# Performance work log

Hardware: AMD Instinct MI355X
Metric: run time of the kernel (lower is better)

The kernel has to match this reference:

```python
import jax, jax.numpy as jnp
import numpy as np

N_NODES = 20000
N_EDGES = 320000
IN_DIM = 256
HIDDEN = 256
OUT_DIM = 128
N_LAYERS = 3
N_GROUPS = 4
EXP_PER_GROUP = 2
N_EXPERTS = N_GROUPS * EXP_PER_GROUP
TOP_K = 2


def setup_inputs() -> dict:
    key = jax.random.key(0)
    ks = jax.random.split(key, 12)
    d = HIDDEN
    r = 2 * d  # router/expert input dim: concat(node, neighbor-mean)
    x = jax.random.normal(ks[0], (N_NODES, IN_DIM), dtype=jnp.float32)
    edge_index = jax.random.randint(ks[1], (2, N_EDGES), 0, N_NODES, dtype=jnp.int32)
    s = 0.05
    Wg = jax.random.normal(ks[2], (N_LAYERS, r, N_GROUPS), dtype=jnp.float32) * s
    We = jax.random.normal(ks[3], (N_LAYERS, r, N_EXPERTS), dtype=jnp.float32) * s
    Ww = jax.random.normal(ks[4], (N_LAYERS, r, d), dtype=jnp.float32) * s
    W1 = jax.random.normal(ks[5], (N_LAYERS, N_EXPERTS, r, d), dtype=jnp.float32) * s
    b1 = jnp.zeros((N_LAYERS, N_EXPERTS, d), dtype=jnp.float32)
    W2 = jax.random.normal(ks[6], (N_LAYERS, N_EXPERTS, d, d), dtype=jnp.float32) * s
    b2 = jnp.zeros((N_LAYERS, N_EXPERTS, d), dtype=jnp.float32)
    wc = jax.random.normal(ks[7], (N_LAYERS, r, 1), dtype=jnp.float32) * s
    Wout = jax.random.normal(ks[8], (d, OUT_DIM), dtype=jnp.float32) * s
    return {"x": x, "edge_index": edge_index, "Wg": Wg, "We": We, "Ww": Ww,
            "W1": W1, "b1": b1, "W2": W2, "b2": b2, "wc": wc, "Wout": Wout}


def _moe_layer(h, src, dst, deg, Wg, We, Ww, W1, b1, W2, b2, wc):
    N = h.shape[0]
    # graph message passing: mean aggregation over incoming edges
    agg = jax.ops.segment_sum(h[src], dst, num_segments=N) / deg  # [N, d]
    r = jnp.concatenate([h, agg], axis=-1)  # [N, 2d] combined router input
    # hierarchical routing: group softmax x within-group expert softmax
    gp = jax.nn.softmax(r @ Wg, axis=-1)                                # [N, G]
    ep = jax.nn.softmax((r @ We).reshape(N, N_GROUPS, EXP_PER_GROUP), axis=-1)
    probs = (gp[..., None] * ep).reshape(N, N_EXPERTS)                  # [N, E]
    # top-k gating, renormalized
    topv, topi = jax.lax.top_k(probs, TOP_K)
    gates = jnp.zeros_like(probs).at[jnp.arange(N)[:, None], topi].set(topv)
    gates = gates / (gates.sum(-1, keepdims=True) + 1e-9)              # [N, E]
    # strong experts: per-expert 2-layer MLP, combined by gates
    hid = jax.nn.relu(jnp.einsum('nf,efd->ned', r, W1) + b1[None])      # [N, E, d]
    exp_out = jnp.einsum('ned,edo->neo', hid, W2) + b2[None]            # [N, E, d]
    strong = jnp.einsum('ne,neo->no', gates, exp_out)                   # [N, d]
    # weak shared expert + confidence gate blend
    weak = r @ Ww                                                       # [N, d]
    conf = jax.nn.sigmoid(r @ wc)                                       # [N, 1]
    return jax.nn.relu(conf * strong + (1.0 - conf) * weak)


def reference(x, edge_index, Wg, We, Ww, W1, b1, W2, b2, wc, Wout):
    src, dst = edge_index[0], edge_index[1]
    N = x.shape[0]
    deg = jax.ops.segment_sum(jnp.ones((edge_index.shape[1],), jnp.float32), dst,
                              num_segments=N)
    deg = jnp.maximum(deg, 1.0)[:, None]
    h = x
    for l in range(Wg.shape[0]):  # small fixed layer loop
        h = _moe_layer(h, src, dst, deg, Wg[l], We[l], Ww[l],
                       W1[l], b1[l], W2[l], b2[l], wc[l])
    return h @ Wout
```

## Files before the change

kernel.cpp:

```cpp
#include <hip/hip_runtime.h>

#define NN 20000
#define NEDGE 320000
#define D 256
#define RD 512
#define OD 128
#define NEXP 8
#define NSLOT (2*NN)
#define NODE_BLOCKS 79
#define ASSIGN_BLOCKS 157

typedef unsigned short u16;
typedef __attribute__((ext_vector_type(4))) short short4v;
typedef __attribute__((ext_vector_type(8))) short short8v;
typedef __attribute__((ext_vector_type(16))) float f32x16;

__device__ __forceinline__ void split1(float v, u16& h, u16& m, u16& l) {
    unsigned b = __float_as_uint(v);
    h = (u16)(b >> 16);
    float fh = __uint_as_float(b & 0xffff0000u);
    float r1 = v - fh;
    unsigned b1 = __float_as_uint(r1);
    m = (u16)(b1 >> 16);
    float fm = __uint_as_float(b1 & 0xffff0000u);
    float r2 = r1 - fm;
    l = (u16)(__float_as_uint(r2) >> 16);
}


__global__ void copy_x_zero_cnt_k(const float* __restrict__ x, float* __restrict__ r,
                                  int* __restrict__ cnt) {
    int gid = blockIdx.x * 256 + threadIdx.x;
    int n = gid >> 6;
    int c4 = gid & 63;
    if (gid < NN * (D / 4)) {
        float4 v = reinterpret_cast<const float4*>(x)[gid];
        reinterpret_cast<float4*>(r + (size_t)n * RD)[c4] = v;
    }
    if (gid < NN) cnt[gid] = 0;
}

__global__ void count_edges_k(const int* __restrict__ dst, int* __restrict__ cnt) {
    int e = blockIdx.x * 256 + threadIdx.x;
    if (e < NEDGE) atomicAdd(&cnt[dst[e]], 1);
}

__global__ void block_sums_k(const int* __restrict__ cnt, int* __restrict__ bsum) {
    __shared__ int s[256];
    int i = blockIdx.x * 256 + threadIdx.x;
    s[threadIdx.x] = (i < NN) ? cnt[i] : 0;
    __syncthreads();
    for (int off = 128; off > 0; off >>= 1) {
        if (threadIdx.x < off) s[threadIdx.x] += s[threadIdx.x + off];
        __syncthreads();
    }
    if (threadIdx.x == 0) bsum[blockIdx.x] = s[0];
}

__global__ void scan_bsums_k(int* __restrict__ bsum, int* __restrict__ row_start) {
    if (blockIdx.x == 0 && threadIdx.x == 0) {
        int acc = 0;
        for (int i = 0; i < NODE_BLOCKS; i++) { int t = bsum[i]; bsum[i] = acc; acc += t; }
        row_start[NN] = acc;
    }
}

__global__ void block_scan_k(const int* __restrict__ cnt, const int* __restrict__ bsum,
                             int* __restrict__ row_start, int* __restrict__ cur) {
    __shared__ int s[256];
    int i = blockIdx.x * 256 + threadIdx.x;
    int v = (i < NN) ? cnt[i] : 0;
    s[threadIdx.x] = v;
    __syncthreads();
    for (int off = 1; off < 256; off <<= 1) {
        int t = (threadIdx.x >= off) ? s[threadIdx.x - off] : 0;
        __syncthreads();
        s[threadIdx.x] += t;
        __syncthreads();
    }
    int excl = s[threadIdx.x] - v + bsum[blockIdx.x];
    if (i < NN) { row_start[i] = excl; cur[i] = excl; }
}

__global__ void fill_csr_k(const int* __restrict__ src, const int* __restrict__ dst,
                           int* __restrict__ cur, int* __restrict__ csr_src) {
    int e = blockIdx.x * 256 + threadIdx.x;
    if (e < NEDGE) {
        int pos = atomicAdd(&cur[dst[e]], 1);
        csr_src[pos] = src[e];
    }
}

__global__ void aggregate_k(float* __restrict__ r, const int* __restrict__ row_start,
                            const int* __restrict__ csr_src, int* __restrict__ ec) {
    if (blockIdx.x == 0 && threadIdx.x < 16) ec[threadIdx.x] = 0;
    int wid = blockIdx.x * 4 + (threadIdx.x >> 6);
    int lane = threadIdx.x & 63;
    if (wid >= NN) return;
    int beg = row_start[wid], end = row_start[wid + 1];
    float ax = 0.f, ay = 0.f, az = 0.f, aw = 0.f;
    for (int j = beg; j < end; j++) {
        int s = csr_src[j];
        float4 v = reinterpret_cast<const float4*>(r + (size_t)s * RD)[lane];
        ax += v.x; ay += v.y; az += v.z; aw += v.w;
    }
    float deg = (float)((end - beg) > 1 ? (end - beg) : 1);
    float4 o = make_float4(ax / deg, ay / deg, az / deg, aw / deg);
    reinterpret_cast<float4*>(r + (size_t)wid * RD + D)[lane] = o;
}

__global__ void router_k(const float* __restrict__ r, const float* __restrict__ Wg,
                         const float* __restrict__ We, const float* __restrict__ wc,
                         int* __restrict__ node_top, float* __restrict__ node_gate,
                         float* __restrict__ conf) {
    int wid = blockIdx.x * 4 + (threadIdx.x >> 6);
    int lane = threadIdx.x & 63;
    if (wid >= NN) return;

    const float* rrow = r + (size_t)wid * RD;
    float pg[4] = {0, 0, 0, 0};
    float pe[8] = {0, 0, 0, 0, 0, 0, 0, 0};
    float pc = 0.f;
#pragma unroll
    for (int i = 0; i < 8; i++) {
        int k = lane + i * 64;
        float rv = rrow[k];
        float4 wg = *reinterpret_cast<const float4*>(Wg + (size_t)k * 4);
        pg[0] = fmaf(rv, wg.x, pg[0]); pg[1] = fmaf(rv, wg.y, pg[1]);
        pg[2] = fmaf(rv, wg.z, pg[2]); pg[3] = fmaf(rv, wg.w, pg[3]);
        float4 w0 = *reinterpret_cast<const float4*>(We + (size_t)k * 8);
        float4 w1 = *reinterpret_cast<const float4*>(We + (size_t)k * 8 + 4);
        pe[0] = fmaf(rv, w0.x, pe[0]); pe[1] = fmaf(rv, w0.y, pe[1]);
        pe[2] = fmaf(rv, w0.z, pe[2]); pe[3] = fmaf(rv, w0.w, pe[3]);
        pe[4] = fmaf(rv, w1.x, pe[4]); pe[5] = fmaf(rv, w1.y, pe[5]);
        pe[6] = fmaf(rv, w1.z, pe[6]); pe[7] = fmaf(rv, w1.w, pe[7]);
        pc = fmaf(rv, wc[k], pc);
    }
#pragma unroll
    for (int off = 32; off > 0; off >>= 1) {
#pragma unroll
        for (int g = 0; g < 4; g++) pg[g] += __shfl_xor(pg[g], off);
#pragma unroll
        for (int g = 0; g < 8; g++) pe[g] += __shfl_xor(pe[g], off);
        pc += __shfl_xor(pc, off);
    }

    if (lane == 0) {
        float m = fmaxf(fmaxf(pg[0], pg[1]), fmaxf(pg[2], pg[3]));
        float eg[4]; float sg = 0.f;
#pragma unroll
        for (int g = 0; g < 4; g++) { eg[g] = expf(pg[g] - m); sg += eg[g]; }
        float probs[8];
#pragma unroll
        for (int g = 0; g < 4; g++) {
            float a = pe[2 * g], b = pe[2 * g + 1];
            float mm = fmaxf(a, b);
            float ea = expf(a - mm), eb = expf(b - mm);
            float inv = 1.f / (ea + eb);
            float gp = eg[g] / sg;
            probs[2 * g]     = gp * ea * inv;
            probs[2 * g + 1] = gp * eb * inv;
        }
        int i0 = 0; float v0 = probs[0];
#pragma unroll
        for (int j = 1; j < 8; j++) if (probs[j] > v0) { v0 = probs[j]; i0 = j; }
        int i1 = -1; float v1 = -1e30f;
#pragma unroll
        for (int j = 0; j < 8; j++) if (j != i0 && probs[j] > v1) { v1 = probs[j]; i1 = j; }
        float s = v0 + v1 + 1e-9f;
        node_top[2 * wid] = i0;  node_top[2 * wid + 1] = i1;
        node_gate[2 * wid] = v0 / s;  node_gate[2 * wid + 1] = v1 / s;
        conf[wid] = 1.f / (1.f + expf(-pc));
    }
}

__global__ void expert_hist_k(const int* __restrict__ node_top, int* __restrict__ ec) {
    __shared__ int h[NEXP];
    if (threadIdx.x < NEXP) h[threadIdx.x] = 0;
    __syncthreads();
    int i = blockIdx.x * 256 + threadIdx.x;
    if (i < NSLOT) atomicAdd(&h[node_top[i]], 1);
    __syncthreads();
    if (threadIdx.x < NEXP && h[threadIdx.x] > 0) atomicAdd(&ec[threadIdx.x], h[threadIdx.x]);
}

__global__ void expert_scan_k(const int* __restrict__ ec, int* __restrict__ es,
                              int* __restrict__ ecur) {
    if (blockIdx.x == 0 && threadIdx.x == 0) {
        int acc = 0;
        for (int e = 0; e < NEXP; e++) { es[e] = acc; acc += ec[e]; ecur[e] = 0; }
        es[NEXP] = acc;
    }
}

__global__ void fill_experts_k(const int* __restrict__ node_top, const float* __restrict__ node_gate,
                               const int* __restrict__ es, int* __restrict__ ecur,
                               int* __restrict__ slot_node, float* __restrict__ slot_gate,
                               int* __restrict__ node_slot) {
    __shared__ int hcnt[NEXP], hbase[NEXP];
    int tid = threadIdx.x;
    if (tid < NEXP) hcnt[tid] = 0;
    __syncthreads();
    int i = blockIdx.x * 256 + tid;
    int e = 0, local = 0;
    bool act = (i < NSLOT);
    if (act) {
        e = node_top[i];
        local = atomicAdd(&hcnt[e], 1);
    }
    __syncthreads();
    if (tid < NEXP) hbase[tid] = (hcnt[tid] > 0) ? atomicAdd(&ecur[tid], hcnt[tid]) : 0;
    __syncthreads();
    if (act) {
        int slot = es[e] + hbase[e] + local;
        slot_node[slot] = i >> 1;
        slot_gate[slot] = node_gate[i];
        node_slot[i] = slot;
    }
}

__global__ void combine_k(const float* __restrict__ expout, const float* __restrict__ weak,
                          const float* __restrict__ conf, const int* __restrict__ node_slot,
                          float* __restrict__ r) {
    int gid = blockIdx.x * 256 + threadIdx.x;
    if (gid >= NN * (D / 4)) return;
    int n = gid >> 6, c4 = gid & 63;
    int s0 = node_slot[2 * n], s1 = node_slot[2 * n + 1];
    float4 e0 = reinterpret_cast<const float4*>(expout + (size_t)s0 * D)[c4];
    float4 e1 = reinterpret_cast<const float4*>(expout + (size_t)s1 * D)[c4];
    float4 w  = reinterpret_cast<const float4*>(weak + (size_t)n * D)[c4];
    float cf = conf[n], cg = 1.f - cf;
    float4 o;
    o.x = fmaxf(cf * (e0.x + e1.x) + cg * w.x, 0.f);
    o.y = fmaxf(cf * (e0.y + e1.y) + cg * w.y, 0.f);
    o.z = fmaxf(cf * (e0.z + e1.z) + cg * w.z, 0.f);
    o.w = fmaxf(cf * (e0.w + e1.w) + cg * w.w, 0.f);
    reinterpret_cast<float4*>(r + (size_t)n * RD)[c4] = o;
}

__global__ void btile_k(const float* __restrict__ src, u16* __restrict__ dH,
                        u16* __restrict__ dM, u16* __restrict__ dL,
                        int K, int N, int total) {
    int gid = blockIdx.x * 256 + threadIdx.x;
    if (gid >= total) return;
    int l = gid & 63;
    int tile = gid >> 6;
    int K16 = K >> 4;
    int kb = tile % K16;
    int t2 = tile / K16;
    int N32 = N >> 5;
    int nb = t2 % N32;
    int mat = t2 / N32;
    int kbase = (kb << 4) + ((l >> 5) << 3);
    int n = (nb << 5) + (l & 31);
    const float* s = src + ((size_t)mat * K + kbase) * N + n;
    short8v vh, vm, vl;
#pragma unroll
    for (int j = 0; j < 8; j++) {
        u16 hh, mm, ll;
        split1(s[(size_t)j * N], hh, mm, ll);
        vh[j] = (short)hh; vm[j] = (short)mm; vl[j] = (short)ll;
    }
    size_t o = (size_t)gid * 8;
    *reinterpret_cast<short8v*>(dH + o) = vh;
    *reinterpret_cast<short8v*>(dM + o) = vm;
    *reinterpret_cast<short8v*>(dL + o) = vl;
}

template <int MODE>
__global__ __launch_bounds__(256, 5) void gemm_mfma(
    const float* __restrict__ A, int lda,
    const u16* __restrict__ BH, const u16* __restrict__ BM,
    const u16* __restrict__ BL,
    const float* __restrict__ bias,
    float* __restrict__ C, int ldc,
    const int* __restrict__ es,
    const int* __restrict__ slot_node,
    const float* __restrict__ slot_gate,
    int M, int N, int K) {
    constexpr int PL2 = 1024;
    __shared__ u16 sA[3 * PL2];

    int tid = threadIdx.x;
    int row0, valid_rows;
    if (MODE == 0) {
        row0 = blockIdx.x * 64;
        valid_rows = M - row0; if (valid_rows > 64) valid_rows = 64;
    } else {
        int bx = blockIdx.x, acc0 = 0, expert = -1, mt = 0;
        row0 = 0; valid_rows = 0;
        for (int e = 0; e < NEXP; e++) {
            int c = es[e + 1] - es[e];
            int t = (c + 63) >> 6;
            if (bx < acc0 + t) {
                expert = e; mt = bx - acc0; row0 = es[e] + (mt << 6);
                valid_rows = c - (mt << 6); if (valid_rows > 64) valid_rows = 64;
                break;
            }
            acc0 += t;
        }
        if (expert < 0) return;
        int bo = expert * N * K;
        BH += bo; BM += bo; BL += bo;
        bias += expert * D;
    }
    int ncol0 = blockIdx.y * 128;

    int srow = tid >> 2;
    int koff = (tid & 3) * 4;
    int grow;
    {
        int i0 = row0 + srow;
        if (MODE == 1) {
            i0 = i0 < NSLOT ? i0 : NSLOT - 1;
            grow = slot_node[i0];
        } else {
            grow = i0 < M ? i0 : M - 1;
        }
    }
    const float* pA = A + (size_t)grow * lda + koff;
    int woff = ((srow >> 5) * 2 + (koff >> 3)) * 256 + (srow & 31) * 8 + (koff & 4);

    int lane = tid & 63;
    int wave = tid >> 6;
    int wr = (wave & 1) * 32;
    int wc = (wave >> 1) * 64;
    int fl = lane & 31;
    int K16 = K >> 4;
    int nb0 = (ncol0 + wc) >> 5;
    int tbase0 = nb0 * K16 * 512 + lane * 8;
    int tbase1 = (nb0 + 1) * K16 * 512 + lane * 8;
    int roff = ((wr >> 5) * 2 + (lane >> 5)) * 256 + fl * 8;

    f32x16 acc0 = {};
    f32x16 acc1 = {};

    for (int kt = 0; kt < K; kt += 16) {
        float4 av = *reinterpret_cast<const float4*>(pA + kt);
        int ko = (kt >> 4) * 512;
        short8v bH0 = *reinterpret_cast<const short8v*>(BH + tbase0 + ko);
        short8v bM0 = *reinterpret_cast<const short8v*>(BM + tbase0 + ko);
        short8v bL0 = *reinterpret_cast<const short8v*>(BL + tbase0 + ko);
        short8v bH1 = *reinterpret_cast<const short8v*>(BH + tbase1 + ko);
        short8v bM1 = *reinterpret_cast<const short8v*>(BM + tbase1 + ko);
        short8v bL1 = *reinterpret_cast<const short8v*>(BL + tbase1 + ko);
        __syncthreads();
        {
            u16 h0, m0, l0, h1, m1, l1, h2, m2, l2, h3, m3, l3;
            split1(av.x, h0, m0, l0);
            split1(av.y, h1, m1, l1);
            split1(av.z, h2, m2, l2);
            split1(av.w, h3, m3, l3);
            short4v hv = {(short)h0, (short)h1, (short)h2, (short)h3};
            short4v mv = {(short)m0, (short)m1, (short)m2, (short)m3};
            short4v lv = {(short)l0, (short)l1, (short)l2, (short)l3};
            *reinterpret_cast<short4v*>(&sA[0 * PL2 + woff]) = hv;
            *reinterpret_cast<short4v*>(&sA[1 * PL2 + woff]) = mv;
            *reinterpret_cast<short4v*>(&sA[2 * PL2 + woff]) = lv;
        }
        __syncthreads();
        short8v aH = *reinterpret_cast<const short8v*>(&sA[0 * PL2 + roff]);
        short8v aM = *reinterpret_cast<const short8v*>(&sA[1 * PL2 + roff]);
        short8v aL = *reinterpret_cast<const short8v*>(&sA[2 * PL2 + roff]);
#define MFMA_ACC(d, a, b) d = __builtin_amdgcn_mfma_f32_32x32x16_bf16(a, b, d, 0, 0, 0)
        MFMA_ACC(acc0, aH, bH0); MFMA_ACC(acc0, aH, bM0);
        MFMA_ACC(acc0, aM, bH0); MFMA_ACC(acc0, aH, bL0);
        MFMA_ACC(acc0, aM, bM0); MFMA_ACC(acc0, aL, bH0);
        MFMA_ACC(acc1, aH, bH1); MFMA_ACC(acc1, aH, bM1);
        MFMA_ACC(acc1, aM, bH1); MFMA_ACC(acc1, aH, bL1);
        MFMA_ACC(acc1, aM, bM1); MFMA_ACC(acc1, aL, bH1);
#undef MFMA_ACC
    }

    int fh = lane >> 5;
#pragma unroll
    for (int j = 0; j < 2; j++) {
        const f32x16& a = j ? acc1 : acc0;
        int colg = ncol0 + wc + j * 32 + fl;
        float bv = (MODE != 0) ? bias[colg] : 0.f;
#pragma unroll
        for (int rg = 0; rg < 16; rg++) {
            int lrow = wr + (rg & 3) + 8 * (rg >> 2) + 4 * fh;
            if (lrow >= valid_rows) continue;
            int growo = row0 + lrow;
            float v = a[rg] + bv;
            if (MODE == 1) {
                v = fmaxf(v, 0.f);
            } else if (MODE == 2) {
                v *= slot_gate[growo];
            }
            C[(size_t)growo * ldc + colg] = v;
        }
    }
}

extern "C" void kernel_launch(void* const* d_in, const int* in_sizes, int n_in,
                              void* d_out, int out_size, void* d_ws, size_t ws_size,
                              hipStream_t stream) {
    (void)in_sizes; (void)n_in; (void)out_size; (void)ws_size;
    const float* x    = (const float*)d_in[0];
    const int*   ei   = (const int*)d_in[1];
    const float* Wg   = (const float*)d_in[2];
    const float* We   = (const float*)d_in[3];
    const float* Ww   = (const float*)d_in[4];
    const float* W1   = (const float*)d_in[5];
    const float* b1   = (const float*)d_in[6];
    const float* W2   = (const float*)d_in[7];
    const float* b2   = (const float*)d_in[8];
    const float* wcp  = (const float*)d_in[9];
    const float* Wout = (const float*)d_in[10];
    float* out = (float*)d_out;

    char* p = (char*)d_ws;
    auto alloc = [&](size_t bytes) -> char* {
        char* q = p; p += (bytes + 255) & ~(size_t)255; return q;
    };
    int*   cnt       = (int*)alloc((size_t)NN * 4);
    int*   row_start = (int*)alloc((size_t)(NN + 1) * 4);
    int*   cur       = (int*)alloc((size_t)NN * 4);
    int*   bsum      = (int*)alloc(128 * 4);
    int*   csr_src   = (int*)alloc((size_t)NEDGE * 4);
    float* r         = (float*)alloc((size_t)NN * RD * 4);
    float* hid       = (float*)alloc((size_t)NSLOT * D * 4);
    float* expout    = (float*)alloc((size_t)NSLOT * D * 4);
    float* conf      = (float*)alloc((size_t)NN * 4);
    int*   node_top  = (int*)alloc((size_t)2 * NN * 4);
    float* node_gate = (float*)alloc((size_t)2 * NN * 4);
    int*   node_slot = (int*)alloc((size_t)2 * NN * 4);
    int*   slot_node = (int*)alloc((size_t)NSLOT * 4);
    float* slot_gate = (float*)alloc((size_t)NSLOT * 4);
    int*   ec        = (int*)alloc(64 * 4);
    int*   es        = (int*)alloc(64 * 4);
    int*   ecur      = (int*)alloc(64 * 4);
    u16* w1tH = (u16*)alloc((size_t)NEXP * D * RD * 2);
    u16* w1tM = (u16*)alloc((size_t)NEXP * D * RD * 2);
    u16* w1tL = (u16*)alloc((size_t)NEXP * D * RD * 2);
    u16* w2tH = (u16*)alloc((size_t)NEXP * D * D * 2);
    u16* w2tM = (u16*)alloc((size_t)NEXP * D * D * 2);
    u16* w2tL = (u16*)alloc((size_t)NEXP * D * D * 2);
    u16* wwtH = (u16*)alloc((size_t)D * RD * 2);
    u16* wwtM = (u16*)alloc((size_t)D * RD * 2);
    u16* wwtL = (u16*)alloc((size_t)D * RD * 2);
    u16* wotH = (u16*)alloc((size_t)OD * D * 2);
    u16* wotM = (u16*)alloc((size_t)OD * D * 2);
    u16* wotL = (u16*)alloc((size_t)OD * D * 2);
    float* weak = hid;

    const int* srcp = ei;
    const int* dstp = ei + NEDGE;
    const int EB = (NEDGE + 255) / 256;

    copy_x_zero_cnt_k<<<5000, 256, 0, stream>>>(x, r, cnt);
    count_edges_k<<<EB, 256, 0, stream>>>(dstp, cnt);
    block_sums_k<<<NODE_BLOCKS, 256, 0, stream>>>(cnt, bsum);
    scan_bsums_k<<<1, 64, 0, stream>>>(bsum, row_start);
    block_scan_k<<<NODE_BLOCKS, 256, 0, stream>>>(cnt, bsum, row_start, cur);
    fill_csr_k<<<EB, 256, 0, stream>>>(srcp, dstp, cur, csr_src);
    btile_k<<<16, 256, 0, stream>>>(Wout, wotH, wotM, wotL, D, OD, 4096);

    for (int l = 0; l < 3; l++) {
        btile_k<<<512, 256, 0, stream>>>(W1 + (size_t)l * NEXP * RD * D,
                                         w1tH, w1tM, w1tL, RD, D, 131072);
        btile_k<<<256, 256, 0, stream>>>(W2 + (size_t)l * NEXP * D * D,
                                         w2tH, w2tM, w2tL, D, D, 65536);
        btile_k<<<64, 256, 0, stream>>>(Ww + (size_t)l * RD * D,
                                        wwtH, wwtM, wwtL, RD, D, 16384);
        aggregate_k<<<5000, 256, 0, stream>>>(r, row_start, csr_src, ec);
        router_k<<<5000, 256, 0, stream>>>(r,
            Wg + (size_t)l * RD * 4, We + (size_t)l * RD * 8, wcp + (size_t)l * RD,
            node_top, node_gate, conf);
        expert_hist_k<<<ASSIGN_BLOCKS, 256, 0, stream>>>(node_top, ec);
        expert_scan_k<<<1, 64, 0, stream>>>(ec, es, ecur);
        fill_experts_k<<<ASSIGN_BLOCKS, 256, 0, stream>>>(node_top, node_gate, es, ecur,
                                                          slot_node, slot_gate, node_slot);
        gemm_mfma<1><<<dim3(640, 2), 256, 0, stream>>>(r, RD, w1tH, w1tM, w1tL,
            b1 + (size_t)l * NEXP * D, hid, D, es, slot_node, slot_gate, NSLOT, D, RD);
        gemm_mfma<2><<<dim3(640, 2), 256, 0, stream>>>(hid, D, w2tH, w2tM, w2tL,
            b2 + (size_t)l * NEXP * D, expout, D, es, slot_node, slot_gate, NSLOT, D, D);
        gemm_mfma<0><<<dim3(313, 2), 256, 0, stream>>>(r, RD, wwtH, wwtM, wwtL,
            nullptr, weak, D, nullptr, nullptr, nullptr, NN, D, RD);
        combine_k<<<5000, 256, 0, stream>>>(expout, weak, conf, node_slot, r);
    }
    gemm_mfma<0><<<dim3(313, 1), 256, 0, stream>>>(r, RD, wotH, wotM, wotL,
        nullptr, out, OD, nullptr, nullptr, nullptr, NN, OD, D);
}
```

Baseline: 825.3 us.

## Load A fragments directly per lane, drop shared-memory staging and barriers

After: 915.0 us. 1.11x slower.

```diff
diff --git a/kernel.cpp b/kernel.cpp
--- a/kernel.cpp
+++ b/kernel.cpp
@@ -11,7 +11,6 @@
 #define ASSIGN_BLOCKS 157
 
 typedef unsigned short u16;
-typedef __attribute__((ext_vector_type(4))) short short4v;
 typedef __attribute__((ext_vector_type(8))) short short8v;
 typedef __attribute__((ext_vector_type(16))) float f32x16;
 
@@ -25,6 +24,17 @@
     float fm = __uint_as_float(b1 & 0xffff0000u);
     float r2 = r1 - fm;
     l = (u16)(__float_as_uint(r2) >> 16);
+}
+
+__device__ __forceinline__ void split8(const float4& x, const float4& y,
+                                       short8v& h, short8v& m, short8v& l) {
+    float v[8] = {x.x, x.y, x.z, x.w, y.x, y.y, y.z, y.w};
+#pragma unroll
+    for (int i = 0; i < 8; i++) {
+        u16 hh, mm, ll;
+        split1(v[i], hh, mm, ll);
+        h[i] = (short)hh; m[i] = (short)mm; l[i] = (short)ll;
+    }
 }
 
 
@@ -278,9 +288,6 @@
     const int* __restrict__ slot_node,
     const float* __restrict__ slot_gate,
     int M, int N, int K) {
-    constexpr int PL2 = 1024;
-    __shared__ u16 sA[3 * PL2];
-
     int tid = threadIdx.x;
     int row0, valid_rows;
     if (MODE == 0) {
@@ -306,37 +313,37 @@
     }
     int ncol0 = blockIdx.y * 128;
 
-    int srow = tid >> 2;
-    int koff = (tid & 3) * 4;
-    int grow;
-    {
-        int i0 = row0 + srow;
-        if (MODE == 1) {
-            i0 = i0 < NSLOT ? i0 : NSLOT - 1;
-            grow = slot_node[i0];
-        } else {
-            grow = i0 < M ? i0 : M - 1;
-        }
-    }
-    const float* pA = A + (size_t)grow * lda + koff;
-    int woff = ((srow >> 5) * 2 + (koff >> 3)) * 256 + (srow & 31) * 8 + (koff & 4);
-
     int lane = tid & 63;
     int wave = tid >> 6;
     int wr = (wave & 1) * 32;
     int wc = (wave >> 1) * 64;
     int fl = lane & 31;
+    int kh8 = (lane >> 5) * 8;
+
+    int arow;
+    {
+        int i0 = row0 + wr + fl;
+        if (MODE == 1) {
+            i0 = i0 < NSLOT ? i0 : NSLOT - 1;
+            arow = slot_node[i0];
+        } else {
+            arow = i0 < M ? i0 : M - 1;
+        }
+    }
+    const float* pA = A + (size_t)arow * lda + kh8;
+
     int K16 = K >> 4;
     int nb0 = (ncol0 + wc) >> 5;
     int tbase0 = nb0 * K16 * 512 + lane * 8;
     int tbase1 = (nb0 + 1) * K16 * 512 + lane * 8;
-    int roff = ((wr >> 5) * 2 + (lane >> 5)) * 256 + fl * 8;
 
     f32x16 acc0 = {};
     f32x16 acc1 = {};
 
+#pragma unroll 2
     for (int kt = 0; kt < K; kt += 16) {
-        float4 av = *reinterpret_cast<const float4*>(pA + kt);
+        float4 a0 = *reinterpret_cast<const float4*>(pA + kt);
+        float4 a1 = *reinterpret_cast<const float4*>(pA + kt + 4);
         int ko = (kt >> 4) * 512;
         short8v bH0 = *reinterpret_cast<const short8v*>(BH + tbase0 + ko);
         short8v bM0 = *reinterpret_cast<const short8v*>(BM + tbase0 + ko);
@@ -344,24 +351,8 @@
         short8v bH1 = *reinterpret_cast<const short8v*>(BH + tbase1 + ko);
         short8v bM1 = *reinterpret_cast<const short8v*>(BM + tbase1 + ko);
         short8v bL1 = *reinterpret_cast<const short8v*>(BL + tbase1 + ko);
-        __syncthreads();
-        {
-            u16 h0, m0, l0, h1, m1, l1, h2, m2, l2, h3, m3, l3;
-            split1(av.x, h0, m0, l0);
-            split1(av.y, h1, m1, l1);
-            split1(av.z, h2, m2, l2);
-            split1(av.w, h3, m3, l3);
-            short4v hv = {(short)h0, (short)h1, (short)h2, (short)h3};
-            short4v mv = {(short)m0, (short)m1, (short)m2, (short)m3};
-            short4v lv = {(short)l0, (short)l1, (short)l2, (short)l3};
-            *reinterpret_cast<short4v*>(&sA[0 * PL2 + woff]) = hv;
-            *reinterpret_cast<short4v*>(&sA[1 * PL2 + woff]) = mv;
-            *reinterpret_cast<short4v*>(&sA[2 * PL2 + woff]) = lv;
-        }
-        __syncthreads();
-        short8v aH = *reinterpret_cast<const short8v*>(&sA[0 * PL2 + roff]);
-        short8v aM = *reinterpret_cast<const short8v*>(&sA[1 * PL2 + roff]);
-        short8v aL = *reinterpret_cast<const short8v*>(&sA[2 * PL2 + roff]);
+        short8v aH, aM, aL;
+        split8(a0, a1, aH, aM, aL);
 #define MFMA_ACC(d, a, b) d = __builtin_amdgcn_mfma_f32_32x32x16_bf16(a, b, d, 0, 0, 0)
         MFMA_ACC(acc0, aH, bH0); MFMA_ACC(acc0, aH, bM0);
         MFMA_ACC(acc0, aM, bH0); MFMA_ACC(acc0, aH, bL0);
```

## Fuse weak GEMM into expert GEMM, scatter-add strong output, merge weight tiling

Applied to the files above, without the earlier changes.

Result: slower. 859.8 us (median of 2 runs) (+4.2%).

```diff
diff --git a/kernel.cpp b/kernel.cpp
--- a/kernel.cpp
+++ b/kernel.cpp
@@ -9,6 +9,7 @@
 #define NSLOT (2*NN)
 #define NODE_BLOCKS 79
 #define ASSIGN_BLOCKS 157
+#define EXP_BLOCKS 640
 
 typedef unsigned short u16;
 typedef __attribute__((ext_vector_type(4))) short short4v;
@@ -91,9 +92,13 @@
     }
 }
 
+__global__ void zero_k(float* __restrict__ p, int n4) {
+    int i = blockIdx.x * 256 + threadIdx.x;
+    if (i < n4) reinterpret_cast<float4*>(p)[i] = make_float4(0.f, 0.f, 0.f, 0.f);
+}
+
 __global__ void aggregate_k(float* __restrict__ r, const int* __restrict__ row_start,
-                            const int* __restrict__ csr_src, int* __restrict__ ec) {
-    if (blockIdx.x == 0 && threadIdx.x < 16) ec[threadIdx.x] = 0;
+                            const int* __restrict__ csr_src) {
     int wid = blockIdx.x * 4 + (threadIdx.x >> 6);
     int lane = threadIdx.x & 63;
     if (wid >= NN) return;
@@ -174,29 +179,36 @@
     }
 }
 
-__global__ void expert_hist_k(const int* __restrict__ node_top, int* __restrict__ ec) {
+__global__ void hist_part_k(const int* __restrict__ node_top, int* __restrict__ part) {
     __shared__ int h[NEXP];
     if (threadIdx.x < NEXP) h[threadIdx.x] = 0;
     __syncthreads();
     int i = blockIdx.x * 256 + threadIdx.x;
     if (i < NSLOT) atomicAdd(&h[node_top[i]], 1);
     __syncthreads();
-    if (threadIdx.x < NEXP && h[threadIdx.x] > 0) atomicAdd(&ec[threadIdx.x], h[threadIdx.x]);
-}
-
-__global__ void expert_scan_k(const int* __restrict__ ec, int* __restrict__ es,
-                              int* __restrict__ ecur) {
-    if (blockIdx.x == 0 && threadIdx.x == 0) {
+    if (threadIdx.x < NEXP) part[blockIdx.x * NEXP + threadIdx.x] = h[threadIdx.x];
+}
+
+__global__ void scan2_k(const int* __restrict__ part, int* __restrict__ es,
+                        int* __restrict__ ecur) {
+    __shared__ int tot[NEXP];
+    if (threadIdx.x < NEXP) {
+        int s = 0;
+        for (int b = 0; b < ASSIGN_BLOCKS; b++) s += part[b * NEXP + threadIdx.x];
+        tot[threadIdx.x] = s;
+        ecur[threadIdx.x] = 0;
+    }
+    __syncthreads();
+    if (threadIdx.x == 0) {
         int acc = 0;
-        for (int e = 0; e < NEXP; e++) { es[e] = acc; acc += ec[e]; ecur[e] = 0; }
+        for (int e = 0; e < NEXP; e++) { es[e] = acc; acc += tot[e]; }
         es[NEXP] = acc;
     }
 }
 
 __global__ void fill_experts_k(const int* __restrict__ node_top, const float* __restrict__ node_gate,
                                const int* __restrict__ es, int* __restrict__ ecur,
-                               int* __restrict__ slot_node, float* __restrict__ slot_gate,
-                               int* __restrict__ node_slot) {
+                               int* __restrict__ slot_node, float* __restrict__ slot_gate) {
     __shared__ int hcnt[NEXP], hbase[NEXP];
     int tid = threadIdx.x;
     if (tid < NEXP) hcnt[tid] = 0;
@@ -215,34 +227,28 @@
         int slot = es[e] + hbase[e] + local;
         slot_node[slot] = i >> 1;
         slot_gate[slot] = node_gate[i];
-        node_slot[i] = slot;
-    }
-}
-
-__global__ void combine_k(const float* __restrict__ expout, const float* __restrict__ weak,
-                          const float* __restrict__ conf, const int* __restrict__ node_slot,
-                          float* __restrict__ r) {
+    }
+}
+
+__global__ void combine_k(const float* __restrict__ strong, const float* __restrict__ weak,
+                          const float* __restrict__ conf, float* __restrict__ r) {
     int gid = blockIdx.x * 256 + threadIdx.x;
     if (gid >= NN * (D / 4)) return;
     int n = gid >> 6, c4 = gid & 63;
-    int s0 = node_slot[2 * n], s1 = node_slot[2 * n + 1];
-    float4 e0 = reinterpret_cast<const float4*>(expout + (size_t)s0 * D)[c4];
-    float4 e1 = reinterpret_cast<const float4*>(expout + (size_t)s1 * D)[c4];
-    float4 w  = reinterpret_cast<const float4*>(weak + (size_t)n * D)[c4];
+    float4 e = reinterpret_cast<const float4*>(strong + (size_t)n * D)[c4];
+    float4 w = reinterpret_cast<const float4*>(weak + (size_t)n * D)[c4];
     float cf = conf[n], cg = 1.f - cf;
     float4 o;
-    o.x = fmaxf(cf * (e0.x + e1.x) + cg * w.x, 0.f);
-    o.y = fmaxf(cf * (e0.y + e1.y) + cg * w.y, 0.f);
-    o.z = fmaxf(cf * (e0.z + e1.z) + cg * w.z, 0.f);
-    o.w = fmaxf(cf * (e0.w + e1.w) + cg * w.w, 0.f);
+    o.x = fmaxf(cf * e.x + cg * w.x, 0.f);
+    o.y = fmaxf(cf * e.y + cg * w.y, 0.f);
+    o.z = fmaxf(cf * e.z + cg * w.z, 0.f);
+    o.w = fmaxf(cf * e.w + cg * w.w, 0.f);
     reinterpret_cast<float4*>(r + (size_t)n * RD)[c4] = o;
 }
 
-__global__ void btile_k(const float* __restrict__ src, u16* __restrict__ dH,
-                        u16* __restrict__ dM, u16* __restrict__ dL,
-                        int K, int N, int total) {
-    int gid = blockIdx.x * 256 + threadIdx.x;
-    if (gid >= total) return;
+__device__ __forceinline__ void btile_one(const float* __restrict__ src,
+                                          u16* __restrict__ dH, u16* __restrict__ dM,
+                                          u16* __restrict__ dL, int K, int N, int gid) {
     int l = gid & 63;
     int tile = gid >> 6;
     int K16 = K >> 4;
@@ -267,6 +273,30 @@
     *reinterpret_cast<short8v*>(dL + o) = vl;
 }
 
+__global__ void btile_k(const float* __restrict__ src, u16* __restrict__ dH,
+                        u16* __restrict__ dM, u16* __restrict__ dL,
+                        int K, int N, int total) {
+    int gid = blockIdx.x * 256 + threadIdx.x;
+    if (gid >= total) return;
+    btile_one(src, dH, dM, dL, K, N, gid);
+}
+
+__global__ void btile3_k(const float* __restrict__ s1, u16* __restrict__ aH,
+                         u16* __restrict__ aM, u16* __restrict__ aL,
+                         const float* __restrict__ s2, u16* __restrict__ bH,
+                         u16* __restrict__ bM, u16* __restrict__ bL,
+                         const float* __restrict__ s3, u16* __restrict__ cH,
+                         u16* __restrict__ cM, u16* __restrict__ cL) {
+    int gid = blockIdx.x * 256 + threadIdx.x;
+    if (gid < 131072) {
+        btile_one(s1, aH, aM, aL, RD, D, gid);
+    } else if (gid < 131072 + 65536) {
+        btile_one(s2, bH, bM, bL, D, D, gid - 131072);
+    } else if (gid < 131072 + 65536 + 16384) {
+        btile_one(s3, cH, cM, cL, RD, D, gid - 131072 - 65536);
+    }
+}
+
 template <int MODE>
 __global__ __launch_bounds__(256, 5) void gemm_mfma(
     const float* __restrict__ A, int lda,
@@ -277,15 +307,26 @@
     const int* __restrict__ es,
     const int* __restrict__ slot_node,
     const float* __restrict__ slot_gate,
-    int M, int N, int K) {
+    int M, int N, int K,
+    const u16* __restrict__ VH, const u16* __restrict__ VM,
+    const u16* __restrict__ VL, float* __restrict__ Cw,
+    int weak_base, int Mw) {
     constexpr int PL2 = 1024;
     __shared__ u16 sA[3 * PL2];
 
     int tid = threadIdx.x;
     int row0, valid_rows;
+    bool isweak = false;
     if (MODE == 0) {
         row0 = blockIdx.x * 64;
         valid_rows = M - row0; if (valid_rows > 64) valid_rows = 64;
+    } else if (MODE == 1 && (int)blockIdx.x >= weak_base) {
+        isweak = true;
+        row0 = ((int)blockIdx.x - weak_base) * 64;
+        valid_rows = Mw - row0; if (valid_rows > 64) valid_rows = 64;
+        if (valid_rows <= 0) return;
+        BH = VH; BM = VM; BL = VL;
+        C = Cw;
     } else {
         int bx = blockIdx.x, acc0 = 0, expert = -1, mt = 0;
         row0 = 0; valid_rows = 0;
@@ -311,9 +352,13 @@
     int grow;
     {
         int i0 = row0 + srow;
-        if (MODE == 1) {
+        if (MODE == 1 && !isweak) {
             i0 = i0 < NSLOT ? i0 : NSLOT - 1;
             grow = slot_node[i0];
+        } else if (MODE == 2) {
+            grow = i0 < M ? i0 : M - 1;
+        } else if (MODE == 1) {
+            grow = i0 < Mw ? i0 : Mw - 1;
         } else {
             grow = i0 < M ? i0 : M - 1;
         }
@@ -377,19 +422,23 @@
     for (int j = 0; j < 2; j++) {
         const f32x16& a = j ? acc1 : acc0;
         int colg = ncol0 + wc + j * 32 + fl;
-        float bv = (MODE != 0) ? bias[colg] : 0.f;
+        float bv = (MODE != 0 && !isweak) ? bias[colg] : 0.f;
 #pragma unroll
         for (int rg = 0; rg < 16; rg++) {
             int lrow = wr + (rg & 3) + 8 * (rg >> 2) + 4 * fh;
             if (lrow >= valid_rows) continue;
             int growo = row0 + lrow;
             float v = a[rg] + bv;
-            if (MODE == 1) {
+            if (MODE == 1 && !isweak) {
                 v = fmaxf(v, 0.f);
+                C[(size_t)growo * ldc + colg] = v;
             } else if (MODE == 2) {
                 v *= slot_gate[growo];
+                int node = slot_node[growo];
+                atomicAdd(&C[(size_t)node * ldc + colg], v);
+            } else {
+                C[(size_t)growo * ldc + colg] = v;
             }
-            C[(size_t)growo * ldc + colg] = v;
         }
     }
 }
@@ -422,14 +471,14 @@
     int*   csr_src   = (int*)alloc((size_t)NEDGE * 4);
     float* r         = (float*)alloc((size_t)NN * RD * 4);
     float* hid       = (float*)alloc((size_t)NSLOT * D * 4);
-    float* expout    = (float*)alloc((size_t)NSLOT * D * 4);
+    float* strong    = (float*)alloc((size_t)NN * D * 4);
+    float* weak      = (float*)alloc((size_t)NN * D * 4);
     float* conf      = (float*)alloc((size_t)NN * 4);
     int*   node_top  = (int*)alloc((size_t)2 * NN * 4);
     float* node_gate = (float*)alloc((size_t)2 * NN * 4);
-    int*   node_slot = (int*)alloc((size_t)2 * NN * 4);
     int*   slot_node = (int*)alloc((size_t)NSLOT * 4);
     float* slot_gate = (float*)alloc((size_t)NSLOT * 4);
-    int*   ec        = (int*)alloc(64 * 4);
+    int*   part      = (int*)alloc((size_t)ASSIGN_BLOCKS * NEXP * 4);
     int*   es        = (int*)alloc(64 * 4);
     int*   ecur      = (int*)alloc(64 * 4);
     u16* w1tH = (u16*)alloc((size_t)NEXP * D * RD * 2);
@@ -444,7 +493,6 @@
     u16* wotH = (u16*)alloc((size_t)OD * D * 2);
     u16* wotM = (u16*)alloc((size_t)OD * D * 2);
     u16* wotL = (u16*)alloc((size_t)OD * D * 2);
-    float* weak = hid;
 
     const int* srcp = ei;
     const int* dstp = ei + NEDGE;
@@ -459,28 +507,31 @@
     btile_k<<<16, 256, 0, stream>>>(Wout, wotH, wotM, wotL, D, OD, 4096);
 
     for (int l = 0; l < 3; l++) {
-        btile_k<<<512, 256, 0, stream>>>(W1 + (size_t)l * NEXP * RD * D,
-                                         w1tH, w1tM, w1tL, RD, D, 131072);
-        btile_k<<<256, 256, 0, stream>>>(W2 + (size_t)l * NEXP * D * D,
-                                         w2tH, w2tM, w2tL, D, D, 65536);
-        btile_k<<<64, 256, 0, stream>>>(Ww + (size_t)l * RD * D,
-                                        wwtH, wwtM, wwtL, RD, D, 16384);
-        aggregate_k<<<5000, 256, 0, stream>>>(r, row_start, csr_src, ec);
+        btile3_k<<<832, 256, 0, stream>>>(
+            W1 + (size_t)l * NEXP * RD * D, w1tH, w1tM, w1tL,
+            W2 + (size_t)l * NEXP * D * D,  w2tH, w2tM, w2tL,
+            Ww + (size_t)l * RD * D,        wwtH, wwtM, wwtL);
+        aggregate_k<<<5000, 256, 0, stream>>>(r, row_start, csr_src);
         router_k<<<5000, 256, 0, stream>>>(r,
             Wg + (size_t)l * RD * 4, We + (size_t)l * RD * 8, wcp + (size_t)l * RD,
             node_top, node_gate, conf);
-        expert_hist_k<<<ASSIGN_BLOCKS, 256, 0, stream>>>(node_top, ec);
-        expert_scan_k<<<1, 64, 0, stream>>>(ec, es, ecur);
+        hist_part_k<<<ASSIGN_BLOCKS, 256, 0, stream>>>(node_top, part);
+        scan2_k<<<1, 64, 0, stream>>>(part, es, ecur);
         fill_experts_k<<<ASSIGN_BLOCKS, 256, 0, stream>>>(node_top, node_gate, es, ecur,
-                                                          slot_node, slot_gate, node_slot);
-        gemm_mfma<1><<<dim3(640, 2), 256, 0, stream>>>(r, RD, w1tH, w1tM, w1tL,
-            b1 + (size_t)l * NEXP * D, hid, D, es, slot_node, slot_gate, NSLOT, D, RD);
-        gemm_mfma<2><<<dim3(640, 2), 256, 0, stream>>>(hid, D, w2tH, w2tM, w2tL,
-            b2 + (size_t)l * NEXP * D, expout, D, es, slot_node, slot_gate, NSLOT, D, D);
-        gemm_mfma<0><<<dim3(313, 2), 256, 0, stream>>>(r, RD, wwtH, wwtM, wwtL,
-            nullptr, weak, D, nullptr, nullptr, nullptr, NN, D, RD);
-        combine_k<<<5000, 256, 0, stream>>>(expout, weak, conf, node_slot, r);
-    }
-    gemm_mfma<0><<<dim3(313, 1), 256, 0, stream>>>(r, RD, wotH, wotM, wotL,
-        nullptr, out, OD, nullptr, nullptr, nullptr, NN, OD, D);
-}
+                                                          slot_node, slot_gate);
+        zero_k<<<5000, 256, 0, stream>>>(strong, NN * D / 4);
+        gemm_mfma<1><<<dim3(EXP_BLOCKS + 313, 2), 256, 0, stream>>>(
+            r, RD, w1tH, w1tM, w1tL, b1 + (size_t)l * NEXP * D, hid, D,
+            es, slot_node, slot_gate, NSLOT, D, RD,
+            wwtH, wwtM, wwtL, weak, EXP_BLOCKS, NN);
+        gemm_mfma<2><<<dim3(EXP_BLOCKS, 2), 256, 0, stream>>>(
+            hid, D, w2tH, w2tM, w2tL, b2 + (size_t)l * NEXP * D, strong, D,
+            es, slot_node, slot_gate, NSLOT, D, D,
+            nullptr, nullptr, nullptr, nullptr, 1 << 30, 0);
+        combine_k<<<5000, 256, 0, stream>>>(strong, weak, conf, r);
+    }
+    gemm_mfma<0><<<dim3(313, 1), 256, 0, stream>>>(
+        r, RD, wotH, wotM, wotL, nullptr, out, OD,
+        nullptr, nullptr, nullptr, NN, OD, D,
+        nullptr, nullptr, nullptr, nullptr, 1 << 30, 0);
+}
```
